# Kernel optimization log

Measured on AMD Instinct MI355X. Metric: run time of the kernel, lower is better.

Reference implementation:

```python
import jax, jax.numpy as jnp
import numpy as np

NUM_HEADS = 16


def rotary_pos_emb(x):
    # x: [b, h, s, d] with interleaved rotary pairs (d even)
    d, s = x.shape[-1], x.shape[-2]
    ts = jnp.arange(0, d, 2, dtype=jnp.float32)
    inv_freqs = 10000.0 ** (-ts / d)                      # [d/2]
    grid = jnp.arange(s, dtype=jnp.float32)[:, None] * inv_freqs[None, :]  # [s, d/2]
    sin = jnp.repeat(jnp.sin(grid), 2, axis=-1)           # [s, d]
    cos = jnp.repeat(jnp.cos(grid), 2, axis=-1)           # [s, d]
    x1, x2 = x[..., ::2], x[..., 1::2]
    xs = jnp.stack([-x2, x1], axis=-1).reshape(x.shape)   # rotate pairs
    return x * cos + xs * sin


def setup_inputs() -> dict:
    key = jax.random.key(0)
    ks = jax.random.split(key, 6)
    b, l, d = 2, 2048, 1024
    x = jax.random.normal(ks[0], (b, l, d), dtype=jnp.float32)
    # additive causal mask: 0 on/below diag, large negative above
    causal = jnp.tril(jnp.ones((l, l), dtype=bool))
    mask = jnp.where(causal, 0.0, -1e9).astype(jnp.float32)[None, None]  # [1,1,l,l]
    s = 0.01  # VarianceScaling(0.01)-ish small init
    Wq = jax.random.normal(ks[1], (d, d), dtype=jnp.float32) * s
    Wk = jax.random.normal(ks[2], (d, d), dtype=jnp.float32) * s
    Wv = jax.random.normal(ks[3], (d, d), dtype=jnp.float32) * s
    Wo = jax.random.normal(ks[4], (d, d), dtype=jnp.float32) * s
    return {"x": x, "mask": mask, "Wq": Wq, "Wk": Wk, "Wv": Wv, "Wo": Wo}


def reference(x, mask, Wq, Wk, Wv, Wo):
    b, l, d = x.shape
    h = NUM_HEADS
    k_sz = d // h
    split = lambda t: t.reshape(b, l, h, k_sz).transpose(0, 2, 1, 3)  # b h l k
    # NOTE: original scales q by 1/sqrt(model_dim) (not key_size), before RoPE
    q = split(x @ Wq / jnp.sqrt(jnp.float32(d)))
    q = rotary_pos_emb(q)
    k = rotary_pos_emb(split(x @ Wk))
    v = split(x @ Wv)
    logits = jnp.einsum('bhik,bhjk->bhij', q, k) + mask   # [b,h,l,l]
    a = jax.nn.softmax(logits, axis=-1)
    y = jnp.einsum('bhij,bhjv->bhiv', a, v)               # [b,h,l,k]
    y = y.transpose(0, 2, 1, 3).reshape(b, l, d)
    return y @ Wo
```

## Files before the change

kernel.cpp:

```cpp
#include <hip/hip_runtime.h>
#include <math.h>

#define L 2048
#define D 1024
#define H 16
#define KS 64
#define BBATCH 2

typedef float f32x4 __attribute__((ext_vector_type(4)));
typedef short s16x8 __attribute__((ext_vector_type(8)));

__device__ __forceinline__ ushort f2bf(float f) {
    union { float f; unsigned u; } v; v.f = f;
    unsigned lsb = (v.u >> 16) & 1u;
    v.u += 0x7fffu + lsb;
    return (ushort)(v.u >> 16);
}

__device__ __forceinline__ unsigned fbits(float f) {
    union { float f; unsigned u; } v; v.f = f; return v.u;
}

__device__ __forceinline__ void gl_lds16(const ushort* g, ushort* l) {
    __builtin_amdgcn_global_load_lds(
        (const __attribute__((address_space(1))) unsigned int*)g,
        (__attribute__((address_space(3))) unsigned int*)l, 16, 0, 0);
}

__global__ __launch_bounds__(256)
void prep(const float* __restrict__ x,
          const float* __restrict__ W0, const float* __restrict__ W1,
          const float* __restrict__ W2, const float* __restrict__ W3,
          ushort* __restrict__ xb, ushort* __restrict__ Wt,
          float2* __restrict__ tab)
{
    __shared__ float T[32][33];
    const int bid = blockIdx.x;
    const int tid = threadIdx.x;
    if (bid < 4096) {
        const int i = bid * 1024 + tid * 4;
        const float4 v = *(const float4*)&x[i];
        ushort4 p = make_ushort4(f2bf(v.x), f2bf(v.y), f2bf(v.z), f2bf(v.w));
        *(ushort4*)&xb[i] = p;
    } else if (bid < 8192) {
        const int t = bid - 4096;
        const int z = t >> 10;
        const float* W = (z == 0) ? W0 : (z == 1) ? W1 : (z == 2) ? W2 : W3;
        ushort* out = Wt + (size_t)z * D * D;
        const int r0 = ((t >> 5) & 31) * 32, c0 = (t & 31) * 32;
        const int tr = tid >> 3, tc = (tid & 7) * 4;
        const float4 v = *(const float4*)&W[(size_t)(r0 + tr) * D + c0 + tc];
        T[tr][tc + 0] = v.x; T[tr][tc + 1] = v.y;
        T[tr][tc + 2] = v.z; T[tr][tc + 3] = v.w;
        __syncthreads();
        ushort4 p = make_ushort4(f2bf(T[tc + 0][tr]), f2bf(T[tc + 1][tr]),
                                 f2bf(T[tc + 2][tr]), f2bf(T[tc + 3][tr]));
        *(ushort4*)&out[(size_t)(c0 + tr) * D + r0 + tc] = p;
    } else {
        const int idx = (bid - 8192) * 256 + tid;
        const int dd2 = idx >> 11, s = idx & 2047;
        const float inv = __expf(-(float)(2 * dd2) * (9.210340371976184f / 64.0f));
        float sn, cs;
        sincosf((float)s * inv, &sn, &cs);
        tab[idx] = make_float2(cs, sn);
    }
}

__global__ __launch_bounds__(512, 2)
void qkv_gemm(const ushort* __restrict__ A, const ushort* __restrict__ B,
              const float2* __restrict__ tab,
              ushort* __restrict__ Qo, ushort* __restrict__ Ko,
              ushort* __restrict__ Vto)
{
    __shared__ __align__(16) ushort smem[28672];
    const int tid  = threadIdx.x;
    const int wv   = tid >> 6, lane = tid & 63;
    const int i16  = lane & 15, quad = lane >> 4;
    const int wr   = wv >> 2, wc = wv & 3;

    int bid = blockIdx.y * 16 + blockIdx.x;
    bid = (bid & 7) * 32 + (bid >> 3);
    const int by = bid & 15, bx = bid >> 4;
    const int m0 = by * 192, n0 = bx * 256;

    const bool isAw = (wv < 4);
    const int cb = isAw ? tid : (tid - 256);
    const ushort* Mp = isAw ? A : B;
    const int rbase = isAw ? m0 : n0;
    const int lbo   = isAw ? 0 : 6144;
    const int c0 = cb, c1 = 256 + cb, c2 = 512 + cb, c3 = 768 + cb;
    const size_t src0 = (size_t)(rbase + (c0 >> 2)) * D + (((c0 & 3) * 8) ^ (((c0 >> 4) & 3) << 3));
    const size_t src1 = (size_t)(rbase + (c1 >> 2)) * D + (((c1 & 3) * 8) ^ (((c1 >> 4) & 3) << 3));
    const size_t src2 = (size_t)(rbase + (c2 >> 2)) * D + (((c2 & 3) * 8) ^ (((c2 >> 4) & 3) << 3));
    const size_t src3 = (size_t)(rbase + (c3 >> 2)) * D + (((c3 & 3) * 8) ^ (((c3 >> 4) & 3) << 3));
    const int ldo0 = lbo + c0 * 8, ldo1 = lbo + c1 * 8;
    const int ldo2 = lbo + c2 * 8, ldo3 = lbo + c3 * 8;

    f32x4 acc[6][4];
    #pragma unroll
    for (int i = 0; i < 6; ++i)
        #pragma unroll
        for (int j = 0; j < 4; ++j) acc[i][j] = (f32x4){0.f, 0.f, 0.f, 0.f};

#define STAGE(kt) do { ushort* S_ = smem + ((kt) & 1) * 14336;                \
        gl_lds16(Mp + src0 + (size_t)(kt) * 32, S_ + ldo0);                   \
        gl_lds16(Mp + src1 + (size_t)(kt) * 32, S_ + ldo1);                   \
        gl_lds16(Mp + src2 + (size_t)(kt) * 32, S_ + ldo2);                   \
        if (!isAw) gl_lds16(Mp + src3 + (size_t)(kt) * 32, S_ + ldo3); } while (0)

    STAGE(0);
    asm volatile("s_waitcnt vmcnt(0)" ::: "memory");
    __builtin_amdgcn_s_barrier();
    __builtin_amdgcn_sched_barrier(0);

    #pragma unroll 1
    for (int kt = 0; kt < 32; ++kt) {
        const ushort* As = smem + (kt & 1) * 14336;
        const ushort* Bs = As + 6144;
        s16x8 afr[6], bfr[4];

        #pragma unroll
        for (int mf = 0; mf < 6; ++mf) {
            int ad = (wr * 96 + mf * 16 + i16) * 64 + quad * 16;
            ad ^= ((ad >> 8) & 3) << 4;
            afr[mf] = *(const s16x8*)((const char*)As + ad);
        }
        #pragma unroll
        for (int nf = 0; nf < 4; ++nf) {
            int ad = (wc * 64 + nf * 16 + i16) * 64 + quad * 16;
            ad ^= ((ad >> 8) & 3) << 4;
            bfr[nf] = *(const s16x8*)((const char*)Bs + ad);
        }
        if (kt < 31) STAGE(kt + 1);
        #pragma unroll
        for (int mf = 0; mf < 6; ++mf)
            #pragma unroll
            for (int nf = 0; nf < 4; ++nf)
                acc[mf][nf] = __builtin_amdgcn_mfma_f32_16x16x32_bf16(
                    afr[mf], bfr[nf], acc[mf][nf], 0, 0, 0);

        asm volatile("s_waitcnt vmcnt(0)" ::: "memory");
        __builtin_amdgcn_s_barrier();
        __builtin_amdgcn_sched_barrier(0);
    }
#undef STAGE

    const int tbase = n0 + wc * 64;
    ushort* T = smem + wv * 1152;
    #pragma unroll
    for (int mf = 0; mf < 6; ++mf) {
        const int dim0 = m0 + wr * 96 + mf * 16;
        const int region = dim0 >> 10;
        if (region < 2) {
            ushort* out = (region == 0) ? Qo : Ko;
            const bool isQ = (region == 0);
            const int qd = (dim0 & 1023) + quad * 4;
            const int hh = qd >> 6, dd = qd & 63;
            #pragma unroll
            for (int nf = 0; nf < 4; ++nf) {
                const int token = tbase + nf * 16 + i16;
                const int b = token >> 11, s = token & 2047;
                ushort4 p;
                #pragma unroll
                for (int pr = 0; pr < 2; ++pr) {
                    float e = acc[mf][nf][2 * pr];
                    float o = acc[mf][nf][2 * pr + 1];
                    if (isQ) { e *= 0.03125f; o *= 0.03125f; }
                    const float2 cssn = tab[(size_t)((dd >> 1) + pr) * 2048 + s];
                    const float ne = e * cssn.x - o * cssn.y;
                    const float no = o * cssn.x + e * cssn.y;
                    if (pr == 0) { p.x = f2bf(ne); p.y = f2bf(no); }
                    else         { p.z = f2bf(ne); p.w = f2bf(no); }
                }
                *(ushort4*)&out[((size_t)(b * H + hh) * L + s) * KS + dd] = p;
            }
        } else {
            #pragma unroll
            for (int nf = 0; nf < 4; ++nf)
                #pragma unroll
                for (int r = 0; r < 4; ++r)
                    T[(quad * 4 + r) * 72 + nf * 16 + i16] = f2bf(acc[mf][nf][r]);
            __builtin_amdgcn_s_waitcnt(0);
            const int tl0 = (lane & 7) * 8;
            #pragma unroll
            for (int c = 0; c < 2; ++c) {
                const int vl = c * 8 + (lane >> 3);
                const s16x8 val = *(const s16x8*)&T[vl * 72 + tl0];
                const int vdim = (dim0 - 2048) + vl;
                const int hh = vdim >> 6, dd = vdim & 63;
                const int token0 = tbase + tl0;
                const int b = token0 >> 11, s0 = token0 & 2047;
                *(s16x8*)&Vto[((size_t)(b * H + hh) * KS + dd) * L + s0] = val;
            }
            __builtin_amdgcn_s_waitcnt(0);
        }
    }
}

__global__ __launch_bounds__(512)
void oproj_gemm(const ushort* __restrict__ A, const ushort* __restrict__ B,
                float* __restrict__ out)
{
    __shared__ __align__(16) ushort smem[32768];
    const int tid  = threadIdx.x;
    const int wv   = tid >> 6, lane = tid & 63;
    const int i16  = lane & 15, quad = lane >> 4;
    const int wr   = wv >> 2, wc = wv & 3;

    const int bid = blockIdx.y * 8 + blockIdx.x;
    const int bx  = bid & 7, by = bid >> 3;
    const int m0  = by * 128, n0 = bx * 128;

    const int c = tid;
    const size_t sA = (size_t)(m0 + (c >> 2)) * D + (((c & 3) * 8) ^ (((c >> 4) & 3) << 3));
    const size_t sB = (size_t)(n0 + (c >> 2)) * D + (((c & 3) * 8) ^ (((c >> 4) & 3) << 3));
    const int ldo = c * 8;

    f32x4 acc[4][2];
    #pragma unroll
    for (int i = 0; i < 4; ++i)
        #pragma unroll
        for (int j = 0; j < 2; ++j) acc[i][j] = (f32x4){0.f, 0.f, 0.f, 0.f};

#define OSTAGE(kt) do { ushort* S_ = smem + ((kt) & 3) * 8192;                \
        gl_lds16(A + sA + (size_t)(kt) * 32, S_ + ldo);                       \
        gl_lds16(B + sB + (size_t)(kt) * 32, S_ + 4096 + ldo); } while (0)

    OSTAGE(0); OSTAGE(1); OSTAGE(2);
    asm volatile("s_waitcnt vmcnt(4)" ::: "memory");
    __builtin_amdgcn_s_barrier();
    __builtin_amdgcn_sched_barrier(0);

    #pragma unroll 1
    for (int kt = 0; kt < 32; ++kt) {
        const ushort* As = smem + (kt & 3) * 8192;
        const ushort* Bs = As + 4096;
        s16x8 afr[4], bfr[2];
        #pragma unroll
        for (int mf = 0; mf < 4; ++mf) {
            int ad = (wr * 64 + mf * 16 + i16) * 64 + quad * 16;
            ad ^= ((ad >> 8) & 3) << 4;
            afr[mf] = *(const s16x8*)((const char*)As + ad);
        }
        #pragma unroll
        for (int nf = 0; nf < 2; ++nf) {
            int ad = (wc * 32 + nf * 16 + i16) * 64 + quad * 16;
            ad ^= ((ad >> 8) & 3) << 4;
            bfr[nf] = *(const s16x8*)((const char*)Bs + ad);
        }
        if (kt < 29) OSTAGE(kt + 3);
        #pragma unroll
        for (int mf = 0; mf < 4; ++mf)
            #pragma unroll
            for (int nf = 0; nf < 2; ++nf)
                acc[mf][nf] = __builtin_amdgcn_mfma_f32_16x16x32_bf16(
                    afr[mf], bfr[nf], acc[mf][nf], 0, 0, 0);

        if (kt <= 28)      { asm volatile("s_waitcnt vmcnt(4)" ::: "memory"); }
        else if (kt == 29) { asm volatile("s_waitcnt vmcnt(2)" ::: "memory"); }
        else if (kt == 30) { asm volatile("s_waitcnt vmcnt(0)" ::: "memory"); }
        __builtin_amdgcn_s_barrier();
        __builtin_amdgcn_sched_barrier(0);
    }
#undef OSTAGE

    #pragma unroll
    for (int mf = 0; mf < 4; ++mf)
        #pragma unroll
        for (int nf = 0; nf < 2; ++nf) {
            const int od = n0 + wc * 32 + nf * 16 + i16;
            const int tk = m0 + wr * 64 + mf * 16 + quad * 4;
            #pragma unroll
            for (int r = 0; r < 4; ++r)
                out[(size_t)(tk + r) * D + od] = acc[mf][nf][r];
        }
}

__global__ __launch_bounds__(512)
void attn_mfma(const ushort* __restrict__ Q, const ushort* __restrict__ K,
               const ushort* __restrict__ Vt, ushort* __restrict__ Yb)
{
    const int bh   = blockIdx.y;
    const int qt   = (bh < 16) ? (15 - blockIdx.x) : blockIdx.x;
    const int tid  = threadIdx.x;
    const int wave = tid >> 6, lane = tid & 63;
    const int i16  = lane & 15, quad = lane >> 4;
    const int r0   = qt * 128 + wave * 16;
    const int row  = r0 + i16;
    const int jtmax = (r0 + 15) >> 6;
    const int jtend = 2 * qt + 1;

    __shared__ __align__(16) ushort Ks[2][64 * 64];
    __shared__ __align__(16) ushort Vs[2][64 * 64];
    __shared__ __align__(16) ushort Ps[8][16 * 72];

    const ushort* Qb = Q  + (size_t)bh * L * KS;
    const ushort* Kb = K  + (size_t)bh * L * KS;
    const ushort* Vb = Vt + (size_t)bh * KS * L;

    const s16x8 qf0 = *(const s16x8*)(Qb + (size_t)row * KS + quad * 8);
    const s16x8 qf1 = *(const s16x8*)(Qb + (size_t)row * KS + 32 + quad * 8);

    const int srow = tid >> 3;
    const int scol = ((tid & 7) ^ ((tid >> 3) & 7)) * 8;
    ushort* kd0 = &Ks[0][0] + tid * 8;
    ushort* vd0 = &Vs[0][0] + tid * 8;
    ushort* kd1 = &Ks[1][0] + tid * 8;
    ushort* vd1 = &Vs[1][0] + tid * 8;

    gl_lds16(Kb + (size_t)srow * KS + scol, kd0);
    gl_lds16(Vb + (size_t)srow * L + scol, vd0);
    asm volatile("s_waitcnt vmcnt(0)" ::: "memory");
    __builtin_amdgcn_s_barrier();

    f32x4 O0 = {0.f,0.f,0.f,0.f}, O1 = O0, O2 = O0, O3 = O0;
    float psum = 0.0f;
    const int xk = (i16 & 7) << 4;

    #pragma unroll 1
    for (int jt = 0; jt <= jtend; ++jt) {
        const int cur = jt & 1;
        const bool has_next = (jt < jtend);

        if (has_next) {
            const int j0n = (jt + 1) * 64;
            gl_lds16(Kb + (size_t)(j0n + srow) * KS + scol, cur ? kd0 : kd1);
            gl_lds16(Vb + (size_t)srow * L + j0n + scol,    cur ? vd0 : vd1);
        }

        if (jt <= jtmax) {
            const int j0 = jt * 64;
            const char* Ksb = (const char*)&Ks[cur][0];
            const char* Vsb = (const char*)&Vs[cur][0];
            f32x4 st[4];
            #pragma unroll
            for (int nt = 0; nt < 4; ++nt) {
                const int rb = (nt * 16 + i16) * 128 + quad * 16;
                const s16x8 kf0 = *(const s16x8*)(Ksb + (rb ^ xk));
                const s16x8 kf1 = *(const s16x8*)(Ksb + ((rb + 64) ^ xk));
                f32x4 c = {0.f,0.f,0.f,0.f};
                c = __builtin_amdgcn_mfma_f32_16x16x32_bf16(kf0, qf0, c, 0, 0, 0);
                c = __builtin_amdgcn_mfma_f32_16x16x32_bf16(kf1, qf1, c, 0, 0, 0);
                st[nt] = c;
            }
            if (jt == jtmax) {
                #pragma unroll
                for (int nt = 0; nt < 4; ++nt)
                    #pragma unroll
                    for (int rg = 0; rg < 4; ++rg) {
                        const int j = j0 + nt * 16 + quad * 4 + rg;
                        if (j > row) st[nt][rg] = -1e30f;
                    }
            }
            float pv[4][4];
            #pragma unroll
            for (int nt = 0; nt < 4; ++nt)
                #pragma unroll
                for (int rg = 0; rg < 4; ++rg) {
                    pv[nt][rg] = __expf(st[nt][rg]);
                    psum += pv[nt][rg];
                }
            ushort* P2 = &Ps[wave][0];
            #pragma unroll
            for (int nt = 0; nt < 4; ++nt) {
                uint2 pk;
                pk.x = __builtin_amdgcn_perm(fbits(pv[nt][1]), fbits(pv[nt][0]), 0x07060302u);
                pk.y = __builtin_amdgcn_perm(fbits(pv[nt][3]), fbits(pv[nt][2]), 0x07060302u);
                *(uint2*)(P2 + i16 * 72 + nt * 16 + quad * 4) = pk;
            }
            const s16x8 pf0 = *(const s16x8*)(P2 + i16 * 72 + quad * 8);
            const s16x8 pf1 = *(const s16x8*)(P2 + i16 * 72 + 32 + quad * 8);
            s16x8 v0, v1;
            int vb0 = (0 * 16 + i16) * 128 + quad * 16;
            v0 = *(const s16x8*)(Vsb + (vb0 ^ xk));
            v1 = *(const s16x8*)(Vsb + ((vb0 + 64) ^ xk));
            O0 = __builtin_amdgcn_mfma_f32_16x16x32_bf16(v0, pf0, O0, 0, 0, 0);
            O0 = __builtin_amdgcn_mfma_f32_16x16x32_bf16(v1, pf1, O0, 0, 0, 0);
            vb0 = (1 * 16 + i16) * 128 + quad * 16;
            v0 = *(const s16x8*)(Vsb + (vb0 ^ xk));
            v1 = *(const s16x8*)(Vsb + ((vb0 + 64) ^ xk));
            O1 = __builtin_amdgcn_mfma_f32_16x16x32_bf16(v0, pf0, O1, 0, 0, 0);
            O1 = __builtin_amdgcn_mfma_f32_16x16x32_bf16(v1, pf1, O1, 0, 0, 0);
            vb0 = (2 * 16 + i16) * 128 + quad * 16;
            v0 = *(const s16x8*)(Vsb + (vb0 ^ xk));
            v1 = *(const s16x8*)(Vsb + ((vb0 + 64) ^ xk));
            O2 = __builtin_amdgcn_mfma_f32_16x16x32_bf16(v0, pf0, O2, 0, 0, 0);
            O2 = __builtin_amdgcn_mfma_f32_16x16x32_bf16(v1, pf1, O2, 0, 0, 0);
            vb0 = (3 * 16 + i16) * 128 + quad * 16;
            v0 = *(const s16x8*)(Vsb + (vb0 ^ xk));
            v1 = *(const s16x8*)(Vsb + ((vb0 + 64) ^ xk));
            O3 = __builtin_amdgcn_mfma_f32_16x16x32_bf16(v0, pf0, O3, 0, 0, 0);
            O3 = __builtin_amdgcn_mfma_f32_16x16x32_bf16(v1, pf1, O3, 0, 0, 0);
        }

        if (has_next) {
            asm volatile("s_waitcnt vmcnt(0)" ::: "memory");
            __builtin_amdgcn_s_barrier();
        }
    }

    psum += __shfl_xor(psum, 16);
    psum += __shfl_xor(psum, 32);
    const float inv_l = __builtin_amdgcn_rcpf(psum);
    const int b = bh >> 4, hh = bh & 15;
    ushort* Yp = Yb + ((size_t)(b * L + row)) * D + hh * KS + quad * 4;
    f32x4 r;
    r = O0 * inv_l; *(ushort4*)(Yp +  0) = make_ushort4(f2bf(r[0]),f2bf(r[1]),f2bf(r[2]),f2bf(r[3]));
    r = O1 * inv_l; *(ushort4*)(Yp + 16) = make_ushort4(f2bf(r[0]),f2bf(r[1]),f2bf(r[2]),f2bf(r[3]));
    r = O2 * inv_l; *(ushort4*)(Yp + 32) = make_ushort4(f2bf(r[0]),f2bf(r[1]),f2bf(r[2]),f2bf(r[3]));
    r = O3 * inv_l; *(ushort4*)(Yp + 48) = make_ushort4(f2bf(r[0]),f2bf(r[1]),f2bf(r[2]),f2bf(r[3]));
}

extern "C" void kernel_launch(void* const* d_in, const int* in_sizes, int n_in,
                              void* d_out, int out_size, void* d_ws, size_t ws_size,
                              hipStream_t stream)
{
    const float* x  = (const float*)d_in[0];
    const float* Wq = (const float*)d_in[2];
    const float* Wk = (const float*)d_in[3];
    const float* Wv = (const float*)d_in[4];
    const float* Wo = (const float*)d_in[5];

    const size_t NTOK = (size_t)BBATCH * L;
    const size_t SZ   = NTOK * D;
    ushort* xb  = (ushort*)d_ws;
    ushort* Wt  = xb + SZ;
    ushort* Qb  = Wt + 4 * (size_t)D * D;
    ushort* Kb  = Qb + SZ;
    ushort* Vtb = Kb + SZ;
    ushort* Yb  = Vtb + SZ;
    float2* tab = (float2*)Yb;

    prep<<<dim3(8448), dim3(256), 0, stream>>>(x, Wq, Wk, Wv, Wo, xb, Wt, tab);

    qkv_gemm<<<dim3(16, 16), dim3(512), 0, stream>>>(Wt, xb, tab, Qb, Kb, Vtb);

    attn_mfma<<<dim3(16, 32), dim3(512), 0, stream>>>(Qb, Kb, Vtb, Yb);

    oproj_gemm<<<dim3(8, 32), dim3(512), 0, stream>>>(Yb, Wt + 3 * (size_t)D * D,
                                                      (float*)d_out);
}
```

Baseline: 187.8 us.

## Double K-tile depth in QKV GEMM and split main loop into four interleaved phases

The QKV projection GEMM now stages 64-wide K tiles instead of 32-wide, halving the number of main-loop iterations, and doubles shared memory with an 8-way XOR swizzle to match. Each iteration is split into four quadrant phases that interleave LDS fragment reads, global-to-LDS prefetches and MFMA bursts, separated by barriers and with raised wave priority during the MFMA sections. Launch bounds drop to one block per CU, so the kernel trades occupancy for fewer synchronisations and better overlap of loads with compute.

```diff
diff --git a/kernel.cpp b/kernel.cpp
--- a/kernel.cpp
+++ b/kernel.cpp
@@ -66,13 +66,13 @@
     }
 }
 
-__global__ __launch_bounds__(512, 2)
+__global__ __launch_bounds__(512, 1)
 void qkv_gemm(const ushort* __restrict__ A, const ushort* __restrict__ B,
               const float2* __restrict__ tab,
               ushort* __restrict__ Qo, ushort* __restrict__ Ko,
               ushort* __restrict__ Vto)
 {
-    __shared__ __align__(16) ushort smem[28672];
+    __shared__ __align__(16) ushort smem[57344];
     const int tid  = threadIdx.x;
     const int wv   = tid >> 6, lane = tid & 63;
     const int i16  = lane & 15, quad = lane >> 4;
@@ -87,14 +87,22 @@
     const int cb = isAw ? tid : (tid - 256);
     const ushort* Mp = isAw ? A : B;
     const int rbase = isAw ? m0 : n0;
-    const int lbo   = isAw ? 0 : 6144;
-    const int c0 = cb, c1 = 256 + cb, c2 = 512 + cb, c3 = 768 + cb;
-    const size_t src0 = (size_t)(rbase + (c0 >> 2)) * D + (((c0 & 3) * 8) ^ (((c0 >> 4) & 3) << 3));
-    const size_t src1 = (size_t)(rbase + (c1 >> 2)) * D + (((c1 & 3) * 8) ^ (((c1 >> 4) & 3) << 3));
-    const size_t src2 = (size_t)(rbase + (c2 >> 2)) * D + (((c2 & 3) * 8) ^ (((c2 >> 4) & 3) << 3));
-    const size_t src3 = (size_t)(rbase + (c3 >> 2)) * D + (((c3 & 3) * 8) ^ (((c3 >> 4) & 3) << 3));
-    const int ldo0 = lbo + c0 * 8, ldo1 = lbo + c1 * 8;
-    const int ldo2 = lbo + c2 * 8, ldo3 = lbo + c3 * 8;
+    const int lbo   = isAw ? 0 : 12288;
+
+#define MKSRC(g) ((size_t)(rbase + ((cb + 256*(g)) >> 3)) * D +               \
+                  (size_t)((((cb + 256*(g)) & 7) * 8) ^ ((((cb + 256*(g)) >> 3) & 7) << 3)))
+#define MKLDO(g) (lbo + (cb + 256*(g)) * 8)
+    const size_t sc0 = MKSRC(0), sc1 = MKSRC(1), sc2 = MKSRC(2);
+    const size_t sc3 = MKSRC(3), sc4 = MKSRC(4), sc5 = MKSRC(5);
+    const size_t sc6 = MKSRC(6), sc7 = MKSRC(7);
+    const int lc0 = MKLDO(0), lc1 = MKLDO(1), lc2 = MKLDO(2);
+    const int lc3 = MKLDO(3), lc4 = MKLDO(4), lc5 = MKLDO(5);
+    const int lc6 = MKLDO(6), lc7 = MKLDO(7);
+#undef MKSRC
+#undef MKLDO
+
+#define STG(kt, S, Lo) gl_lds16(Mp + S + (size_t)(kt) * 64,                   \
+                                smem + ((kt) & 1) * 28672 + Lo)
 
     f32x4 acc[6][4];
     #pragma unroll
@@ -102,48 +110,116 @@
         #pragma unroll
         for (int j = 0; j < 4; ++j) acc[i][j] = (f32x4){0.f, 0.f, 0.f, 0.f};
 
-#define STAGE(kt) do { ushort* S_ = smem + ((kt) & 1) * 14336;                \
-        gl_lds16(Mp + src0 + (size_t)(kt) * 32, S_ + ldo0);                   \
-        gl_lds16(Mp + src1 + (size_t)(kt) * 32, S_ + ldo1);                   \
-        gl_lds16(Mp + src2 + (size_t)(kt) * 32, S_ + ldo2);                   \
-        if (!isAw) gl_lds16(Mp + src3 + (size_t)(kt) * 32, S_ + ldo3); } while (0)
-
-    STAGE(0);
+    STG(0, sc0, lc0); STG(0, sc1, lc1); STG(0, sc2, lc2);
+    STG(0, sc3, lc3); STG(0, sc4, lc4); STG(0, sc5, lc5);
+    if (!isAw) { STG(0, sc6, lc6); STG(0, sc7, lc7); }
     asm volatile("s_waitcnt vmcnt(0)" ::: "memory");
     __builtin_amdgcn_s_barrier();
     __builtin_amdgcn_sched_barrier(0);
 
     #pragma unroll 1
-    for (int kt = 0; kt < 32; ++kt) {
-        const ushort* As = smem + (kt & 1) * 14336;
-        const ushort* Bs = As + 6144;
-        s16x8 afr[6], bfr[4];
-
-        #pragma unroll
-        for (int mf = 0; mf < 6; ++mf) {
-            int ad = (wr * 96 + mf * 16 + i16) * 64 + quad * 16;
-            ad ^= ((ad >> 8) & 3) << 4;
-            afr[mf] = *(const s16x8*)((const char*)As + ad);
-        }
-        #pragma unroll
-        for (int nf = 0; nf < 4; ++nf) {
-            int ad = (wc * 64 + nf * 16 + i16) * 64 + quad * 16;
-            ad ^= ((ad >> 8) & 3) << 4;
-            bfr[nf] = *(const s16x8*)((const char*)Bs + ad);
-        }
-        if (kt < 31) STAGE(kt + 1);
-        #pragma unroll
-        for (int mf = 0; mf < 6; ++mf)
-            #pragma unroll
-            for (int nf = 0; nf < 4; ++nf)
-                acc[mf][nf] = __builtin_amdgcn_mfma_f32_16x16x32_bf16(
-                    afr[mf], bfr[nf], acc[mf][nf], 0, 0, 0);
+    for (int kt = 0; kt < 16; ++kt) {
+        const char* As = (const char*)(smem + (kt & 1) * 28672);
+        const char* Bs = As + 24576;
+        s16x8 a0[6], a1[6], b01[4], b23[4];
+
+        #pragma unroll
+        for (int mf = 0; mf < 3; ++mf)
+            #pragma unroll
+            for (int ks = 0; ks < 2; ++ks) {
+                int ad = (wr * 96 + mf * 16 + i16) * 128 + ks * 64 + quad * 16;
+                ad ^= ((ad >> 7) & 7) << 4;
+                a0[mf * 2 + ks] = *(const s16x8*)(As + ad);
+            }
+        #pragma unroll
+        for (int nf = 0; nf < 2; ++nf)
+            #pragma unroll
+            for (int ks = 0; ks < 2; ++ks) {
+                int ad = (wc * 64 + nf * 16 + i16) * 128 + ks * 64 + quad * 16;
+                ad ^= ((ad >> 7) & 7) << 4;
+                b01[nf * 2 + ks] = *(const s16x8*)(Bs + ad);
+            }
+        if (kt < 15) { STG(kt + 1, sc0, lc0); STG(kt + 1, sc1, lc1); }
+        __builtin_amdgcn_s_barrier();
+        asm volatile("s_waitcnt lgkmcnt(0)" ::: "memory");
+        __builtin_amdgcn_sched_barrier(0);
+        __builtin_amdgcn_s_setprio(1);
+        #pragma unroll
+        for (int mf = 0; mf < 3; ++mf)
+            #pragma unroll
+            for (int nf = 0; nf < 2; ++nf)
+                #pragma unroll
+                for (int ks = 0; ks < 2; ++ks)
+                    acc[mf][nf] = __builtin_amdgcn_mfma_f32_16x16x32_bf16(
+                        a0[mf * 2 + ks], b01[nf * 2 + ks], acc[mf][nf], 0, 0, 0);
+        __builtin_amdgcn_s_setprio(0);
+        __builtin_amdgcn_s_barrier();
+
+        #pragma unroll
+        for (int mf = 0; mf < 3; ++mf)
+            #pragma unroll
+            for (int ks = 0; ks < 2; ++ks) {
+                int ad = (wr * 96 + 48 + mf * 16 + i16) * 128 + ks * 64 + quad * 16;
+                ad ^= ((ad >> 7) & 7) << 4;
+                a1[mf * 2 + ks] = *(const s16x8*)(As + ad);
+            }
+        if (kt < 15) { STG(kt + 1, sc2, lc2); STG(kt + 1, sc3, lc3); }
+        __builtin_amdgcn_s_barrier();
+        asm volatile("s_waitcnt lgkmcnt(0)" ::: "memory");
+        __builtin_amdgcn_sched_barrier(0);
+        __builtin_amdgcn_s_setprio(1);
+        #pragma unroll
+        for (int mf = 0; mf < 3; ++mf)
+            #pragma unroll
+            for (int nf = 0; nf < 2; ++nf)
+                #pragma unroll
+                for (int ks = 0; ks < 2; ++ks)
+                    acc[mf + 3][nf] = __builtin_amdgcn_mfma_f32_16x16x32_bf16(
+                        a1[mf * 2 + ks], b01[nf * 2 + ks], acc[mf + 3][nf], 0, 0, 0);
+        __builtin_amdgcn_s_setprio(0);
+        __builtin_amdgcn_s_barrier();
+
+        #pragma unroll
+        for (int nf = 0; nf < 2; ++nf)
+            #pragma unroll
+            for (int ks = 0; ks < 2; ++ks) {
+                int ad = (wc * 64 + 32 + nf * 16 + i16) * 128 + ks * 64 + quad * 16;
+                ad ^= ((ad >> 7) & 7) << 4;
+                b23[nf * 2 + ks] = *(const s16x8*)(Bs + ad);
+            }
+        if (kt < 15) { STG(kt + 1, sc4, lc4); STG(kt + 1, sc5, lc5); }
+        __builtin_amdgcn_s_barrier();
+        asm volatile("s_waitcnt lgkmcnt(0)" ::: "memory");
+        __builtin_amdgcn_sched_barrier(0);
+        __builtin_amdgcn_s_setprio(1);
+        #pragma unroll
+        for (int mf = 0; mf < 3; ++mf)
+            #pragma unroll
+            for (int nf = 0; nf < 2; ++nf)
+                #pragma unroll
+                for (int ks = 0; ks < 2; ++ks)
+                    acc[mf + 3][nf + 2] = __builtin_amdgcn_mfma_f32_16x16x32_bf16(
+                        a1[mf * 2 + ks], b23[nf * 2 + ks], acc[mf + 3][nf + 2], 0, 0, 0);
+        __builtin_amdgcn_s_setprio(0);
+        __builtin_amdgcn_s_barrier();
+
+        if (kt < 15 && !isAw) { STG(kt + 1, sc6, lc6); STG(kt + 1, sc7, lc7); }
+        __builtin_amdgcn_s_setprio(1);
+        #pragma unroll
+        for (int mf = 0; mf < 3; ++mf)
+            #pragma unroll
+            for (int nf = 0; nf < 2; ++nf)
+                #pragma unroll
+                for (int ks = 0; ks < 2; ++ks)
+                    acc[mf][nf + 2] = __builtin_amdgcn_mfma_f32_16x16x32_bf16(
+                        a0[mf * 2 + ks], b23[nf * 2 + ks], acc[mf][nf + 2], 0, 0, 0);
+        __builtin_amdgcn_s_setprio(0);
 
         asm volatile("s_waitcnt vmcnt(0)" ::: "memory");
         __builtin_amdgcn_s_barrier();
         __builtin_amdgcn_sched_barrier(0);
     }
-#undef STAGE
+#undef STG
 
     const int tbase = n0 + wc * 64;
     ushort* T = smem + wv * 1152;
```

Measured after the change: 180.7 us. 3.8% less time.
